# Optimization experiments

Measured on AMD Instinct MI355X. Metric: run time of the kernel, lower is better.

The kernel has to match this reference:

```python
import jax, jax.numpy as jnp
import numpy as np

EPS = 1e-6
PC_MIN = jnp.array([-50.0, -50.0, -4.0], jnp.float32)
PC_MAX = jnp.array([50.0, 50.0, 4.0], jnp.float32)
IMG_H, IMG_W = 256, 704
G, P, L, D = 1, 8, 4, 128


def _conv3x3(x, w, b):
    y = jax.lax.conv_general_dilated(x, w, (1, 1), ((1, 1), (1, 1)),
                                     dimension_numbers=('NCHW', 'OIHW', 'NCHW'))
    return y + b[None, :, None, None]


def _inorm(x):
    # InstanceNorm2d(affine=False), eps=1e-5, per-sample per-channel over (H,W)
    m = jnp.mean(x, axis=(2, 3), keepdims=True)
    v = jnp.var(x, axis=(2, 3), keepdims=True)
    return (x - m) * jax.lax.rsqrt(v + 1e-5)


def _bilinear(img, xy):
    # img: [H, W, C]; xy: [M, 2] in [0,1] (align_corners=False, zero padding)
    H, W, _ = img.shape
    px = xy[:, 0] * W - 0.5
    py = xy[:, 1] * H - 0.5
    x0 = jnp.floor(px)
    y0 = jnp.floor(py)
    wx = px - x0
    wy = py - y0
    x0 = x0.astype(jnp.int32)
    y0 = y0.astype(jnp.int32)

    def tap(xi, yi, w):
        ok = (xi >= 0) & (xi < W) & (yi >= 0) & (yi < H)
        v = img[jnp.clip(yi, 0, H - 1), jnp.clip(xi, 0, W - 1)]
        return v * (w * ok)[:, None]

    return (tap(x0, y0, (1 - wx) * (1 - wy)) + tap(x0 + 1, y0, wx * (1 - wy)) +
            tap(x0, y0 + 1, (1 - wx) * wy) + tap(x0 + 1, y0 + 1, wx * wy))


def _sampling_4d(pts, feats, scale_w, l2i):
    # pts: [B,Q,G,P,3]; feats: list of [B*G,N,Hl,Wl,C]; scale_w: [B,Q,G,1,P,L]; l2i: [B,N,4,4]
    B, Q, g, p, _ = pts.shape
    N = l2i.shape[1]
    hom = jnp.concatenate([pts, jnp.ones(pts.shape[:-1] + (1,), pts.dtype)], -1)
    cam = jnp.einsum('bnij,bqgpj->bqngpi', l2i, hom)  # project to each camera
    z = cam[..., 2:3]
    xy = cam[..., :2] / jnp.maximum(z, 1e-5)
    xy = xy / jnp.array([IMG_W, IMG_H], xy.dtype)
    xy = jnp.where(z > 1e-5, xy, -1e4)  # behind camera -> samples zero
    xy = jnp.transpose(xy, (0, 3, 2, 1, 4, 5)).reshape(B * g * N, Q * p, 2)
    out = 0.0
    for l, f in enumerate(feats):
        C = f.shape[-1]
        fi = f.reshape(B * g * N, f.shape[2], f.shape[3], C)
        s = jax.vmap(_bilinear)(fi, xy).reshape(B, g, N, Q, p, C).sum(2)  # sum over cameras
        w = jnp.transpose(scale_w[:, :, :, 0, :, l], (0, 2, 1, 3))  # [B,G,Q,P]
        out = out + s * w[..., None]
    return jnp.transpose(out, (0, 2, 1, 3, 4))  # [B,Q,G,P,C]


def _forward(feat0, feat1, feat2, feat3, lidar2img, bev_query, bev_pos,
             in_w, in_b, off_w, off_b, sw_w, sw_b,
             pe_w1, pe_b1, pe_w2, pe_b2,
             mid_w1, mid_b1, mid_w2, mid_b2, mid_w3, mid_b3,
             out_w, out_b):
    B, _, h, w = bev_query.shape
    # decoder prologue: b n (g c) H W -> (b g) n H W c  (G=1)
    feats = [jnp.transpose(f, (0, 1, 3, 4, 2)) for f in (feat0, feat1, feat2, feat3)]
    q = _inorm(bev_query + _conv3x3(bev_query, in_w, in_b))
    qf = jnp.transpose(q, (0, 2, 3, 1)).reshape(B, h * w, D)
    # sampling offsets (1x1 conv as matmul), mode='grid', scale=1.0
    off = jax.nn.sigmoid(qf @ off_w.T + off_b).reshape(B, h * w, G, P, 3)
    lim_xy = 0.25 * 1.0 + EPS
    lim_z = 4.0 + EPS
    off = jnp.concatenate([off[..., :2] * 2 * lim_xy - lim_xy,
                           off[..., 2:3] * 2 * lim_z - lim_z], -1)
    ref = bev_pos.reshape(B, h * w, 1, 1, 3) * (PC_MAX - PC_MIN) + PC_MIN
    pts = ref + off  # [B,Q,G,P,3] in world coords
    sw = (qf @ sw_w.T + sw_b).reshape(B, h * w, G, P, L)[:, :, :, None]  # b q g 1 p l
    sw = jax.nn.softmax(sw, axis=-1)
    sampled = _sampling_4d(pts, feats, sw, lidar2img)  # [B,Q,G,P,128]
    ref_n = (pts - PC_MIN) / (PC_MAX - PC_MIN)
    pe = jax.nn.relu(ref_n @ pe_w1 + pe_b1) @ pe_w2 + pe_b2  # PositionalEncodingMap MLP
    sampled = sampled + pe
    # b (h w) g p c -> b (p g c) h w
    sf = jnp.transpose(sampled, (0, 3, 2, 4, 1)).reshape(B, P * G * 128, h, w)
    m = jax.nn.gelu(jnp.einsum('oi,bihw->bohw', mid_w1, sf) + mid_b1[None, :, None, None], approximate=False)
    m = jax.nn.gelu(jnp.einsum('oi,bihw->bohw', mid_w2, m) + mid_b2[None, :, None, None], approximate=False)
    m = jnp.einsum('oi,bihw->bohw', mid_w3, m) + mid_b3[None, :, None, None]
    q = _inorm(q + m)
    q = _inorm(q + _conv3x3(q, out_w, out_b))
    height = jnp.transpose(off[..., 2], (0, 2, 3, 1)).reshape(B, G, P, h, w)
    return q, height


def _lidar2img_np():
    mats = []
    K = np.array([[500., 0., IMG_W / 2, 0.],
                  [0., 500., IMG_H / 2, 0.],
                  [0., 0., 1., 0.],
                  [0., 0., 0., 1.]])
    for n in range(6):
        th = 2 * np.pi * n / 6
        fwd = np.array([np.cos(th), np.sin(th), 0.])
        right = np.array([-np.sin(th), np.cos(th), 0.])
        down = np.array([0., 0., -1.])
        R = np.stack([right, down, fwd])
        c = fwd * 0.5 + np.array([0., 0., 1.5])
        T = np.eye(4)
        T[:3, :3] = R
        T[:3, 3] = -R @ c
        mats.append(K @ T)
    return np.stack(mats)[None].astype(np.float32)


def setup_inputs():
    key = jax.random.key(0)
    ks = jax.random.split(key, 16)

    def rn(k, shape, s=0.02):
        return jax.random.normal(k, shape, jnp.float32) * s

    B, N, h, w = 1, 6, 128, 128
    return dict(
        feat0=jax.random.normal(ks[0], (B, N, 128, 32, 88), jnp.float32),
        feat1=jax.random.normal(ks[1], (B, N, 128, 16, 44), jnp.float32),
        feat2=jax.random.normal(ks[2], (B, N, 128, 8, 22), jnp.float32),
        feat3=jax.random.normal(ks[3], (B, N, 128, 4, 11), jnp.float32),
        lidar2img=jnp.asarray(_lidar2img_np()),
        bev_query=jax.random.normal(ks[4], (B, 128, h, w), jnp.float32),
        bev_pos=jax.random.uniform(ks[5], (B, h, w, 3), jnp.float32),
        in_w=rn(ks[6], (128, 128, 3, 3)), in_b=jnp.zeros(128, jnp.float32),
        off_w=rn(ks[7], (G * P * 3, 128)),
        off_b=jax.random.uniform(ks[8], (G * P * 3,), jnp.float32, -4.0, 4.0),
        sw_w=rn(ks[9], (G * P * L, 128)), sw_b=jnp.zeros(G * P * L, jnp.float32),
        pe_w1=rn(ks[10], (3, 256), 0.5), pe_b1=jnp.zeros(256, jnp.float32),
        pe_w2=rn(ks[11], (256, 128), 0.1), pe_b2=jnp.zeros(128, jnp.float32),
        mid_w1=rn(ks[12], (512, P * 128)), mid_b1=jnp.zeros(512, jnp.float32),
        mid_w2=rn(ks[13], (512, 512)), mid_b2=jnp.zeros(512, jnp.float32),
        mid_w3=rn(ks[14], (128, 512)), mid_b3=jnp.zeros(128, jnp.float32),
        out_w=rn(ks[15], (128, 128, 3, 3)), out_b=jnp.zeros(128, jnp.float32),
    )


def reference(feat0, feat1, feat2, feat3, lidar2img, bev_query, bev_pos,
              in_w, in_b, off_w, off_b, sw_w, sw_b,
              pe_w1, pe_b1, pe_w2, pe_b2,
              mid_w1, mid_b1, mid_w2, mid_b2, mid_w3, mid_b3,
              out_w, out_b):
    return _forward(feat0, feat1, feat2, feat3, lidar2img, bev_query, bev_pos,
                    in_w, in_b, off_w, off_b, sw_w, sw_b,
                    pe_w1, pe_b1, pe_w2, pe_b2,
                    mid_w1, mid_b1, mid_w2, mid_b2, mid_w3, mid_b3,
                    out_w, out_b)
```

## Files before the change

### kernel.cpp

```cpp
#include <hip/hip_runtime.h>
#include <hip/hip_bf16.h>
#include <math.h>

#define HW 16384

typedef __attribute__((ext_vector_type(8))) short short8;
typedef __attribute__((ext_vector_type(4))) float floatx4;
typedef __attribute__((ext_vector_type(2))) float floatx2;

__device__ __forceinline__ float gelu_exact(float x){
    return 0.5f * x * (1.0f + erff(x * 0.7071067811865475f));
}

__device__ __forceinline__ floatx2 bf2x(unsigned int u){
    floatx2 r;
    r.x = __uint_as_float(u << 16);
    r.y = __uint_as_float(u & 0xffff0000u);
    return r;
}

__global__ __launch_bounds__(256) void feat_transpose_all_k(
    const float* __restrict__ f0, const float* __restrict__ f1,
    const float* __restrict__ f2, const float* __restrict__ f3,
    __hip_bfloat16* __restrict__ out)
{
    int idx = blockIdx.x * 256 + threadIdx.x;
    const float* in; int Hl, Wl, base;
    if (idx < 2162688)      { in = f0; Hl = 32; Wl = 88; base = 0; }
    else if (idx < 2703360) { in = f1; Hl = 16; Wl = 44; base = 2162688; }
    else if (idx < 2838528) { in = f2; Hl = 8;  Wl = 22; base = 2703360; }
    else                    { in = f3; Hl = 4;  Wl = 11; base = 2838528; }
    int r   = idx - base;
    int c   = r & 127;
    int pix = r >> 7;
    int x   = pix % Wl;
    int tt  = pix / Wl;
    int y   = tt % Hl;
    int n   = tt / Hl;
    out[idx] = __float2bfloat16(in[((n * 128 + c) * Hl + y) * Wl + x]);
}

__global__ __launch_bounds__(256) void prep_k(
    const float* __restrict__ mid_w1, const float* __restrict__ mid_w2,
    const float* __restrict__ mid_w3, const float* __restrict__ pe_w2,
    const float* __restrict__ off_w,  const float* __restrict__ off_b,
    const float* __restrict__ sw_w,   const float* __restrict__ sw_b,
    const float* __restrict__ in_w,   const float* __restrict__ out_w,
    __hip_bfloat16* __restrict__ Wb1, __hip_bfloat16* __restrict__ Wb2,
    __hip_bfloat16* __restrict__ Wb3, __hip_bfloat16* __restrict__ Wpe,
    __hip_bfloat16* __restrict__ Wof, float* __restrict__ Bof,
    __hip_bfloat16* __restrict__ Wcv1, __hip_bfloat16* __restrict__ Wcv2)
{
    int b = blockIdx.x, t = threadIdx.x;
    if (b < 2048) {
        int i = b * 256 + t; Wb1[i] = __float2bfloat16(mid_w1[i]);
    } else if (b < 3072) {
        int i = (b - 2048) * 256 + t; Wb2[i] = __float2bfloat16(mid_w2[i]);
    } else if (b < 3328) {
        int i = (b - 3072) * 256 + t; Wb3[i] = __float2bfloat16(mid_w3[i]);
    } else if (b < 3456) {
        int n = b - 3328; Wpe[n * 256 + t] = __float2bfloat16(pe_w2[t * 128 + n]);
    } else if (b < 3584) {
        int n = b - 3456;
        if (t < 128) {
            float w = 0.f;
            if (n < 24)      w = off_w[n * 128 + t];
            else if (n < 56) w = sw_w[(n - 24) * 128 + t];
            Wof[n * 128 + t] = __float2bfloat16(w);
            if (t == 0) Bof[n] = (n < 24) ? off_b[n] : ((n < 56) ? sw_b[n - 24] : 0.f);
        }
    } else if (b < 3712) {
        int o = b - 3584;
        for (int idx = t; idx < 1152; idx += 256) {
            int s = idx >> 7, i = idx & 127;
            Wcv1[o * 1152 + idx] = __float2bfloat16(in_w[(o * 128 + i) * 9 + s]);
        }
    } else {
        int o = b - 3712;
        for (int idx = t; idx < 1152; idx += 256) {
            int s = idx >> 7, i = idx & 127;
            Wcv2[o * 1152 + idx] = __float2bfloat16(out_w[(o * 128 + i) * 9 + s]);
        }
    }
}

__global__ __launch_bounds__(256) void chw2hwc_pad_k(
    const float* __restrict__ q, __hip_bfloat16* __restrict__ out)
{
    __shared__ float tile[128][65];
    int b = blockIdx.x;
    int y = b >> 1, x0 = (b & 1) * 64;
    int t = threadIdx.x;
    int xi = t & 63, c0 = t >> 6;
    for (int c = c0; c < 128; c += 4)
        tile[c][xi] = q[c * HW + y * 128 + x0 + xi];
    __syncthreads();
    int xp = t >> 2, cg = (t & 3) * 32;
    __hip_bfloat16* dst = out + ((size_t)(y + 1) * 130 + (x0 + 1 + xp)) * 128;
    #pragma unroll
    for (int g = 0; g < 4; g++) {
        int c = cg + g * 8;
        union { __hip_bfloat16 h[8]; uint4 u; } pk;
        #pragma unroll
        for (int j = 0; j < 8; j++) pk.h[j] = __float2bfloat16(tile[c + j][xp]);
        *(uint4*)&dst[c] = pk.u;
    }
}

template<int BM, int BN, int ACT, int OUTT, int CONV>
__global__ __launch_bounds__(256) void bgemm_k(
    const __hip_bfloat16* __restrict__ X, const __hip_bfloat16* __restrict__ W,
    const float* __restrict__ bias, void* __restrict__ outp,
    const float* __restrict__ res,
    int M, int K, int N)
{
    constexpr int ROWS = BM + BN;
    __shared__ __align__(16) __hip_bfloat16 SH[ROWS * 32];
    __hip_bfloat16* As = SH;
    __hip_bfloat16* Bs = SH + BM * 32;
    int t = threadIdx.x;
    int w = t >> 6, lane = t & 63;
    int mb = blockIdx.y * BM, nb = blockIdx.x * BN;
    int cy = mb >> 7, cx = mb & 127;
    constexpr int WM = BM / 2;
    constexpr int MI = WM / 16;
    constexpr int NJ = BN / 32;
    int wm = (w & 1) * WM, wn = (w >> 1) * (BN / 2);
    int lm = lane & 15, lq = lane >> 4;
    floatx4 zero = {0.f, 0.f, 0.f, 0.f};
    floatx4 acc[MI][NJ];
    #pragma unroll
    for (int i = 0; i < MI; i++)
        #pragma unroll
        for (int j = 0; j < NJ; j++) acc[i][j] = zero;
    constexpr int ITERS = (ROWS * 4) / 256;
    for (int kb = 0; kb < K; kb += 32) {
        int s = kb >> 7;
        int dyi = s / 3, dxi = s - dyi * 3;
        __syncthreads();
        #pragma unroll
        for (int it = 0; it < ITERS; it++) {
            int chunk = it * 256 + t;
            int row = chunk >> 2, ko = (chunk & 3) * 8;
            const __hip_bfloat16* src;
            if (row < BM) {
                if (CONV)
                    src = X + (((size_t)(cy + dyi) * 130) + (cx + dxi + row)) * 128 + (kb & 127) + ko;
                else
                    src = X + (size_t)(mb + row) * K + kb + ko;
            } else {
                src = W + (size_t)(nb + row - BM) * K + kb + ko;
            }
            __builtin_amdgcn_global_load_lds(
                (const __attribute__((address_space(1))) void*)src,
                (__attribute__((address_space(3))) void*)&SH[(size_t)(it * 256 + (t & ~63)) * 8],
                16, 0, 0);
        }
        __syncthreads();
        short8 af[MI], bf[NJ];
        #pragma unroll
        for (int i = 0; i < MI; i++)
            af[i] = *(const short8*)&As[(wm + i * 16 + lm) * 32 + lq * 8];
        #pragma unroll
        for (int j = 0; j < NJ; j++)
            bf[j] = *(const short8*)&Bs[(wn + j * 16 + lm) * 32 + lq * 8];
        #pragma unroll
        for (int i = 0; i < MI; i++)
            #pragma unroll
            for (int j = 0; j < NJ; j++)
                acc[i][j] = __builtin_amdgcn_mfma_f32_16x16x32_bf16(af[i], bf[j], acc[i][j], 0, 0, 0);
    }
    #pragma unroll
    for (int i = 0; i < MI; i++) {
        #pragma unroll
        for (int j = 0; j < NJ; j++) {
            int n = nb + wn + j * 16 + lm;
            float bv = bias[n];
            #pragma unroll
            for (int r = 0; r < 4; r++) {
                int m = mb + wm + i * 16 + lq * 4 + r;
                float v = acc[i][j][r] + bv;
                if (ACT) v = gelu_exact(v);
                if (OUTT == 0) {
                    ((__hip_bfloat16*)outp)[(size_t)m * N + n] = __float2bfloat16(v);
                } else {
                    if (res) v += res[(size_t)n * M + m];
                    ((float*)outp)[(size_t)n * M + m] = v;
                }
            }
        }
    }
}

__global__ __launch_bounds__(256) void pe_bgemm_k(
    const float* __restrict__ pts, const float* __restrict__ pe_w1,
    const float* __restrict__ pe_b1, const __hip_bfloat16* __restrict__ W,
    const float* __restrict__ bias, __hip_bfloat16* __restrict__ out)
{
    __shared__ __align__(16) __hip_bfloat16 As[128 * 32];
    __shared__ __align__(16) __hip_bfloat16 Bs[128 * 32];
    __shared__ __align__(16) float wps[4][256];
    int t = threadIdx.x;
    int w = t >> 6, lane = t & 63;
    int mb = blockIdx.x * 128;
    {
        int d = t >> 6, c = (t & 63) * 4;
        float4 v;
        if (d == 0) v = *(const float4*)&pe_b1[c];
        else        v = *(const float4*)&pe_w1[(d - 1) * 256 + c];
        *(float4*)&wps[d][c] = v;
    }
    int cg = t & 3;
    int r0 = t >> 2;
    float rn[2][3];
    #pragma unroll
    for (int h = 0; h < 2; h++) {
        int r = mb + r0 + h * 64;
        rn[h][0] = (pts[(size_t)r * 3 + 0] + 50.f) * 0.01f;
        rn[h][1] = (pts[(size_t)r * 3 + 1] + 50.f) * 0.01f;
        rn[h][2] = (pts[(size_t)r * 3 + 2] + 4.f) * 0.125f;
    }
    int wm = (w & 1) * 64, wn = (w >> 1) * 64;
    int lm = lane & 15, lq = lane >> 4;
    floatx4 zero = {0.f, 0.f, 0.f, 0.f};
    floatx4 acc[4][4];
    #pragma unroll
    for (int i = 0; i < 4; i++)
        #pragma unroll
        for (int j = 0; j < 4; j++) acc[i][j] = zero;
    for (int kb = 0; kb < 256; kb += 32) {
        __syncthreads();
        #pragma unroll
        for (int it = 0; it < 2; it++) {
            int chunk = it * 256 + t;
            int brow = chunk >> 2, ko = (chunk & 3) * 8;
            const __hip_bfloat16* src = W + (size_t)brow * 256 + kb + ko;
            __builtin_amdgcn_global_load_lds(
                (const __attribute__((address_space(1))) void*)src,
                (__attribute__((address_space(3))) void*)&Bs[(size_t)(it * 256 + (t & ~63)) * 8],
                16, 0, 0);
        }
        int c0 = kb + cg * 8;
        float4 bva = *(const float4*)&wps[0][c0], bvb = *(const float4*)&wps[0][c0 + 4];
        float4 wxa = *(const float4*)&wps[1][c0], wxb = *(const float4*)&wps[1][c0 + 4];
        float4 wya = *(const float4*)&wps[2][c0], wyb = *(const float4*)&wps[2][c0 + 4];
        float4 wza = *(const float4*)&wps[3][c0], wzb = *(const float4*)&wps[3][c0 + 4];
        #pragma unroll
        for (int h = 0; h < 2; h++) {
            const float* bv = (const float*)&bva;
            const float* wx = (const float*)&wxa;
            const float* wy = (const float*)&wya;
            const float* wz = (const float*)&wza;
            union { __hip_bfloat16 hh[8]; uint4 u; } pk;
            #pragma unroll
            for (int j = 0; j < 4; j++) {
                float v = bv[j] + rn[h][0] * wx[j] + rn[h][1] * wy[j] + rn[h][2] * wz[j];
                pk.hh[j] = __float2bfloat16(fmaxf(v, 0.f));
            }
            bv = (const float*)&bvb; wx = (const float*)&wxb;
            wy = (const float*)&wyb; wz = (const float*)&wzb;
            #pragma unroll
            for (int j = 0; j < 4; j++) {
                float v = bv[j] + rn[h][0] * wx[j] + rn[h][1] * wy[j] + rn[h][2] * wz[j];
                pk.hh[4 + j] = __float2bfloat16(fmaxf(v, 0.f));
            }
            *(uint4*)&As[(r0 + h * 64) * 32 + cg * 8] = pk.u;
        }
        __syncthreads();
        short8 af[4], bf[4];
        #pragma unroll
        for (int i = 0; i < 4; i++)
            af[i] = *(const short8*)&As[(wm + i * 16 + lm) * 32 + lq * 8];
        #pragma unroll
        for (int j = 0; j < 4; j++)
            bf[j] = *(const short8*)&Bs[(wn + j * 16 + lm) * 32 + lq * 8];
        #pragma unroll
        for (int i = 0; i < 4; i++)
            #pragma unroll
            for (int j = 0; j < 4; j++)
                acc[i][j] = __builtin_amdgcn_mfma_f32_16x16x32_bf16(af[i], bf[j], acc[i][j], 0, 0, 0);
    }
    #pragma unroll
    for (int i = 0; i < 4; i++) {
        #pragma unroll
        for (int j = 0; j < 4; j++) {
            int n = wn + j * 16 + lm;
            float bv = bias[n];
            #pragma unroll
            for (int r = 0; r < 4; r++) {
                int m = mb + wm + i * 16 + lq * 4 + r;
                out[(size_t)m * 128 + n] = __float2bfloat16(acc[i][j][r] + bv);
            }
        }
    }
}

__global__ __launch_bounds__(256) void inorm_k(
    const float* __restrict__ a, const float* __restrict__ addc, float* __restrict__ out)
{
    int c = blockIdx.x;
    const float* pa = a + (size_t)c * HW;
    const float* pb = addc ? addc + (size_t)c * HW : nullptr;
    const bool hasb = (pb != nullptr);
    float s = 0.f, s2 = 0.f;
    for (int i = threadIdx.x; i < HW; i += 256) {
        float v = hasb ? (pa[i] + pb[i]) : pa[i];
        s += v; s2 += v * v;
    }
    #pragma unroll
    for (int off = 32; off > 0; off >>= 1) {
        s  += __shfl_down(s,  off);
        s2 += __shfl_down(s2, off);
    }
    __shared__ float ls[4], ls2[4], stats[2];
    int wid = threadIdx.x >> 6, lane = threadIdx.x & 63;
    if (lane == 0) { ls[wid] = s; ls2[wid] = s2; }
    __syncthreads();
    if (threadIdx.x == 0) {
        float t = 0.f, t2 = 0.f;
        for (int i = 0; i < 4; i++) { t += ls[i]; t2 += ls2[i]; }
        float mean = t * (1.0f / HW);
        float var  = t2 * (1.0f / HW) - mean * mean;
        stats[0] = mean;
        stats[1] = rsqrtf(var + 1e-5f);
    }
    __syncthreads();
    float mean = stats[0], rstd = stats[1];
    float* po = out + (size_t)c * HW;
    for (int i = threadIdx.x; i < HW; i += 256) {
        float v = hasb ? (pa[i] + pb[i]) : pa[i];
        po[i] = (v - mean) * rstd;
    }
}

__global__ __launch_bounds__(256) void offpost_k(
    const float* __restrict__ raw, const float* __restrict__ bev_pos,
    float* __restrict__ pts, float* __restrict__ swn, float* __restrict__ height_out)
{
    int pix = blockIdx.x * 256 + threadIdx.x;
    const float pcmin[3] = {-50.f, -50.f, -4.f};
    const float rng[3]   = {100.f, 100.f, 8.f};
    float bp[3];
    #pragma unroll
    for (int d = 0; d < 3; d++) bp[d] = bev_pos[pix * 3 + d];
    #pragma unroll
    for (int p = 0; p < 8; p++) {
        #pragma unroll
        for (int d = 0; d < 3; d++) {
            float acc = raw[(p * 3 + d) * HW + pix];
            float sv = 1.f / (1.f + expf(-acc));
            float lim = (d == 2) ? (4.0f + 1e-6f) : (0.25f + 1e-6f);
            float offv = sv * 2.f * lim - lim;
            float refv = bp[d] * rng[d] + pcmin[d];
            pts[pix * 24 + p * 3 + d] = refv + offv;
            if (d == 2) height_out[p * HW + pix] = offv;
        }
        float r[4], m = -1e30f;
        #pragma unroll
        for (int l = 0; l < 4; l++) {
            r[l] = raw[(24 + p * 4 + l) * HW + pix];
            m = fmaxf(m, r[l]);
        }
        float sum = 0.f;
        #pragma unroll
        for (int l = 0; l < 4; l++) { r[l] = expf(r[l] - m); sum += r[l]; }
        float inv = 1.f / sum;
        #pragma unroll
        for (int l = 0; l < 4; l++) swn[pix * 32 + p * 4 + l] = r[l] * inv;
    }
}

__global__ __launch_bounds__(128) void sample_k(
    const __hip_bfloat16* __restrict__ featT, const float* __restrict__ pts,
    const float* __restrict__ swn,   const float* __restrict__ l2i,
    __hip_bfloat16* __restrict__ sf)
{
    int pix = blockIdx.x;
    int t = threadIdx.x;
    int lane = t & 63, wv = t >> 6;
    __shared__ float pts_s[24];
    __shared__ float swl_s[32];
    __shared__ float M[96];
    __shared__ __align__(16) int   offs[8][24][4];
    __shared__ __align__(16) float wts[8][24][4];
    __shared__ int cnt[8];
    if (t < 96) M[t] = l2i[t];
    if (t < 24) pts_s[t] = pts[pix * 24 + t];
    if (t < 32) swl_s[t] = swn[pix * 32 + t];
    if (t < 8)  cnt[t] = 0;
    __syncthreads();

    floatx2 acc[4];
    #pragma unroll
    for (int i = 0; i < 4; i++) {
        unsigned int u = *(const unsigned int*)&sf[(size_t)pix * 1024 + (wv * 4 + i) * 128 + 2 * lane];
        acc[i] = bf2x(u);
    }

    const int lHt[4] = {32, 16, 8, 4}, lWt[4] = {88, 44, 22, 11};
    const int loff[4] = {0, 2162688, 2703360, 2838528};
    for (int cb = t; cb < 192; cb += 128) {
        int p = cb / 24;
        int rr = cb - p * 24;
        int n = rr >> 2, l = rr & 3;
        float X = pts_s[p * 3], Y = pts_s[p * 3 + 1], Z = pts_s[p * 3 + 2];
        const float* Mn = &M[n * 16];
        float zc = Mn[8] * X + Mn[9] * Y + Mn[10] * Z + Mn[11];
        if (zc > 1e-5f) {
            float inv = 1.f / zc;
            float xn = (Mn[0] * X + Mn[1] * Y + Mn[2] * Z + Mn[3]) * inv * (1.f / 704.f);
            float yn = (Mn[4] * X + Mn[5] * Y + Mn[6] * Z + Mn[7]) * inv * (1.f / 256.f);
            int Wl = lWt[l], Hl = lHt[l];
            float px = xn * Wl - 0.5f, py = yn * Hl - 0.5f;
            px = fminf(fmaxf(px, -2.f), (float)(Wl + 1));
            py = fminf(fmaxf(py, -2.f), (float)(Hl + 1));
            float x0f = floorf(px), y0f = floorf(py);
            float wx = px - x0f, wy = py - y0f;
            int x0 = (int)x0f, y0 = (int)y0f;
            bool xi0 = (unsigned)x0 < (unsigned)Wl, xi1 = (unsigned)(x0 + 1) < (unsigned)Wl;
            bool yi0 = (unsigned)y0 < (unsigned)Hl, yi1 = (unsigned)(y0 + 1) < (unsigned)Hl;
            if ((xi0 || xi1) && (yi0 || yi1)) {
                float wl = swl_s[p * 4 + l];
                float w00 = wl * (1.f - wx) * (1.f - wy) * (float)(xi0 && yi0);
                float w10 = wl * wx * (1.f - wy)         * (float)(xi1 && yi0);
                float w01 = wl * (1.f - wx) * wy         * (float)(xi0 && yi1);
                float w11 = wl * wx * wy                 * (float)(xi1 && yi1);
                int x0c = min(max(x0, 0), Wl - 1), x1c = min(max(x0 + 1, 0), Wl - 1);
                int y0c = min(max(y0, 0), Hl - 1), y1c = min(max(y0 + 1, 0), Hl - 1);
                int base = loff[l] + n * Hl * Wl * 128;
                int idx = atomicAdd(&cnt[p], 1);
                offs[p][idx][0] = base + (y0c * Wl + x0c) * 128;
                offs[p][idx][1] = base + (y0c * Wl + x1c) * 128;
                offs[p][idx][2] = base + (y1c * Wl + x0c) * 128;
                offs[p][idx][3] = base + (y1c * Wl + x1c) * 128;
                wts[p][idx][0] = w00; wts[p][idx][1] = w10;
                wts[p][idx][2] = w01; wts[p][idx][3] = w11;
            }
        }
    }
    __syncthreads();

    #pragma unroll 1
    for (int i = 0; i < 4; i++) {
        int p = wv * 4 + i;
        int np = cnt[p];
        floatx2 a = acc[i];
        #pragma unroll 1
        for (int j = 0; j < np; j++) {
            int4   o = *(const int4*)&offs[p][j][0];
            float4 w = *(const float4*)&wts[p][j][0];
            unsigned int v0 = ((const unsigned int*)(featT + o.x))[lane];
            unsigned int v1 = ((const unsigned int*)(featT + o.y))[lane];
            unsigned int v2 = ((const unsigned int*)(featT + o.z))[lane];
            unsigned int v3 = ((const unsigned int*)(featT + o.w))[lane];
            a += bf2x(v0) * w.x;
            a += bf2x(v1) * w.y;
            a += bf2x(v2) * w.z;
            a += bf2x(v3) * w.w;
        }
        acc[i] = a;
    }
    #pragma unroll
    for (int i = 0; i < 4; i++) {
        union { __hip_bfloat16 h[2]; unsigned int u; } pk;
        pk.h[0] = __float2bfloat16(acc[i].x);
        pk.h[1] = __float2bfloat16(acc[i].y);
        *(unsigned int*)&sf[(size_t)pix * 1024 + (wv * 4 + i) * 128 + 2 * lane] = pk.u;
    }
}

extern "C" void kernel_launch(void* const* d_in, const int* in_sizes, int n_in,
                              void* d_out, int out_size, void* d_ws, size_t ws_size,
                              hipStream_t stream)
{
    const float* feat[4] = {(const float*)d_in[0], (const float*)d_in[1],
                            (const float*)d_in[2], (const float*)d_in[3]};
    const float* l2i       = (const float*)d_in[4];
    const float* bev_query = (const float*)d_in[5];
    const float* bev_pos   = (const float*)d_in[6];
    const float* in_w  = (const float*)d_in[7];  const float* in_b  = (const float*)d_in[8];
    const float* off_w = (const float*)d_in[9];  const float* off_b = (const float*)d_in[10];
    const float* sw_w  = (const float*)d_in[11]; const float* sw_b  = (const float*)d_in[12];
    const float* pe_w1 = (const float*)d_in[13]; const float* pe_b1 = (const float*)d_in[14];
    const float* pe_w2 = (const float*)d_in[15]; const float* pe_b2 = (const float*)d_in[16];
    const float* mid_w1 = (const float*)d_in[17]; const float* mid_b1 = (const float*)d_in[18];
    const float* mid_w2 = (const float*)d_in[19]; const float* mid_b2 = (const float*)d_in[20];
    const float* mid_w3 = (const float*)d_in[21]; const float* mid_b3 = (const float*)d_in[22];
    const float* out_w  = (const float*)d_in[23]; const float* out_b  = (const float*)d_in[24];

    float* ws = (float*)d_ws;
    float* fTf = ws;
    __hip_bfloat16* fT = (__hip_bfloat16*)fTf;
    float* Bb  = fTf + 1436160;
    float* Cb  = Bb + 2097152;
    float* Gb  = Cb + 2097152;
    float* Dp  = Gb + 2097152;
    float* Eb  = Dp + 393216;
    float* QTf = Eb + 524288;
    __hip_bfloat16* qT = (__hip_bfloat16*)QTf;
    float* SFf = QTf + 1081600;
    __hip_bfloat16* sfb = (__hip_bfloat16*)SFf;
    float* M1f = SFf + 8388608;
    __hip_bfloat16* m1b = (__hip_bfloat16*)M1f;
    float* M2f = M1f + 4194304;
    __hip_bfloat16* m2b = (__hip_bfloat16*)M2f;
    float* WC1 = M2f + 4194304;
    __hip_bfloat16* Wcv1 = (__hip_bfloat16*)WC1;
    float* WC2 = WC1 + 73728;
    __hip_bfloat16* Wcv2 = (__hip_bfloat16*)WC2;
    float* W1f = WC2 + 73728;
    __hip_bfloat16* Wb1 = (__hip_bfloat16*)W1f;
    float* W2f = W1f + 262144;
    __hip_bfloat16* Wb2 = (__hip_bfloat16*)W2f;
    float* W3f = W2f + 131072;
    __hip_bfloat16* Wb3 = (__hip_bfloat16*)W3f;
    float* WPf = W3f + 32768;
    __hip_bfloat16* Wpe = (__hip_bfloat16*)WPf;
    float* WOf = WPf + 16384;
    __hip_bfloat16* Wof = (__hip_bfloat16*)WOf;
    float* Bof = WOf + 8192;

    float* q_out = (float*)d_out;
    float* h_out = q_out + 2097152;

    hipMemsetAsync(qT, 0, (size_t)130 * 130 * 128 * sizeof(__hip_bfloat16), stream);

    feat_transpose_all_k<<<11220, 256, 0, stream>>>(feat[0], feat[1], feat[2], feat[3], fT);
    prep_k<<<3840, 256, 0, stream>>>(mid_w1, mid_w2, mid_w3, pe_w2, off_w, off_b, sw_w, sw_b,
                                     in_w, out_w, Wb1, Wb2, Wb3, Wpe, Wof, Bof, Wcv1, Wcv2);

    chw2hwc_pad_k<<<256, 256, 0, stream>>>(bev_query, qT);
    bgemm_k<64, 64, 0, 1, 1><<<dim3(2, 256), 256, 0, stream>>>(qT, Wcv1, in_b, Bb, bev_query, HW, 1152, 128);
    inorm_k<<<128, 256, 0, stream>>>(Bb, nullptr, Cb);

    chw2hwc_pad_k<<<256, 256, 0, stream>>>(Cb, qT);
    bgemm_k<64, 64, 0, 1, 1><<<dim3(2, 256), 256, 0, stream>>>(qT + 131 * 128, Wof, Bof, Bb, nullptr, HW, 128, 128);
    offpost_k<<<64, 256, 0, stream>>>(Bb, bev_pos, Dp, Eb, h_out);

    pe_bgemm_k<<<1024, 256, 0, stream>>>(Dp, pe_w1, pe_b1, Wpe, pe_b2, sfb);

    sample_k<<<HW, 128, 0, stream>>>(fT, Dp, Eb, l2i, sfb);

    bgemm_k<128, 128, 1, 0, 0><<<dim3(4, 128), 256, 0, stream>>>(sfb, Wb1, mid_b1, m1b, nullptr, HW, 1024, 512);
    bgemm_k<128, 128, 1, 0, 0><<<dim3(4, 128), 256, 0, stream>>>(m1b, Wb2, mid_b2, m2b, nullptr, HW, 512, 512);
    bgemm_k<64, 64, 0, 1, 0><<<dim3(2, 256), 256, 0, stream>>>(m2b, Wb3, mid_b3, Bb, Cb, HW, 512, 128);
    inorm_k<<<128, 256, 0, stream>>>(Bb, nullptr, Gb);

    chw2hwc_pad_k<<<256, 256, 0, stream>>>(Gb, qT);
    bgemm_k<64, 64, 0, 1, 1><<<dim3(2, 256), 256, 0, stream>>>(qT, Wcv2, out_b, Cb, Gb, HW, 1152, 128);
    inorm_k<<<128, 256, 0, stream>>>(Cb, nullptr, q_out);
}
```

Before: 442.7 us.

## Fuse instance-norm statistics into GEMM epilogues and widen sampling kernel

The GEMM epilogue now accumulates per-channel sum and sum-of-squares via atomics. Normalization is applied lazily in the following transpose/pad kernel or the residual read, which removes three standalone inorm passes and leaves a cheap vectorized apply only at the end. Separately, sample_k moves to 256 threads per pixel with 2 points per wave and unrolls the tap loop by two for more memory-level parallelism. The trade-off is atomic contention on the stats buffers and E[x²]−mean² variance computed from float atomics, which can be less accurate and order-dependent.

```diff
diff --git a/kernel.cpp b/kernel.cpp
--- a/kernel.cpp
+++ b/kernel.cpp
@@ -85,12 +85,24 @@
 }
 
 __global__ __launch_bounds__(256) void chw2hwc_pad_k(
-    const float* __restrict__ q, __hip_bfloat16* __restrict__ out)
+    const float* __restrict__ q, const float* __restrict__ stats,
+    __hip_bfloat16* __restrict__ out)
 {
     __shared__ float tile[128][65];
+    __shared__ float sm[128], sr[128];
+    int t = threadIdx.x;
+    if (t < 128) {
+        if (stats) {
+            float s = stats[2 * t], s2 = stats[2 * t + 1];
+            float mean = s * (1.0f / HW);
+            sm[t] = mean;
+            sr[t] = rsqrtf(s2 * (1.0f / HW) - mean * mean + 1e-5f);
+        } else {
+            sm[t] = 0.f; sr[t] = 1.f;
+        }
+    }
     int b = blockIdx.x;
     int y = b >> 1, x0 = (b & 1) * 64;
-    int t = threadIdx.x;
     int xi = t & 63, c0 = t >> 6;
     for (int c = c0; c < 128; c += 4)
         tile[c][xi] = q[c * HW + y * 128 + x0 + xi];
@@ -102,7 +114,8 @@
         int c = cg + g * 8;
         union { __hip_bfloat16 h[8]; uint4 u; } pk;
         #pragma unroll
-        for (int j = 0; j < 8; j++) pk.h[j] = __float2bfloat16(tile[c + j][xp]);
+        for (int j = 0; j < 8; j++)
+            pk.h[j] = __float2bfloat16((tile[c + j][xp] - sm[c + j]) * sr[c + j]);
         *(uint4*)&dst[c] = pk.u;
     }
 }
@@ -112,6 +125,7 @@
     const __hip_bfloat16* __restrict__ X, const __hip_bfloat16* __restrict__ W,
     const float* __restrict__ bias, void* __restrict__ outp,
     const float* __restrict__ res,
+    const float* __restrict__ rstats, float* __restrict__ ostats,
     int M, int K, int N)
 {
     constexpr int ROWS = BM + BN;
@@ -170,12 +184,20 @@
             for (int j = 0; j < NJ; j++)
                 acc[i][j] = __builtin_amdgcn_mfma_f32_16x16x32_bf16(af[i], bf[j], acc[i][j], 0, 0, 0);
     }
-    #pragma unroll
-    for (int i = 0; i < MI; i++) {
-        #pragma unroll
-        for (int j = 0; j < NJ; j++) {
-            int n = nb + wn + j * 16 + lm;
-            float bv = bias[n];
+    float invM = 1.0f / (float)M;
+    #pragma unroll
+    for (int j = 0; j < NJ; j++) {
+        int n = nb + wn + j * 16 + lm;
+        float bv = bias[n];
+        float rmean = 0.f, rrstd = 0.f;
+        if (OUTT == 1 && res && rstats) {
+            float s = rstats[2 * n], s2 = rstats[2 * n + 1];
+            rmean = s * invM;
+            rrstd = rsqrtf(s2 * invM - rmean * rmean + 1e-5f);
+        }
+        float ss = 0.f, ss2 = 0.f;
+        #pragma unroll
+        for (int i = 0; i < MI; i++) {
             #pragma unroll
             for (int r = 0; r < 4; r++) {
                 int m = mb + wm + i * 16 + lq * 4 + r;
@@ -184,9 +206,21 @@
                 if (OUTT == 0) {
                     ((__hip_bfloat16*)outp)[(size_t)m * N + n] = __float2bfloat16(v);
                 } else {
-                    if (res) v += res[(size_t)n * M + m];
+                    if (res) {
+                        float rv = res[(size_t)n * M + m];
+                        v += rstats ? (rv - rmean) * rrstd : rv;
+                    }
                     ((float*)outp)[(size_t)n * M + m] = v;
+                    ss += v; ss2 += v * v;
                 }
+            }
+        }
+        if (OUTT == 1 && ostats) {
+            ss  += __shfl_xor(ss, 16);  ss  += __shfl_xor(ss, 32);
+            ss2 += __shfl_xor(ss2, 16); ss2 += __shfl_xor(ss2, 32);
+            if (lq == 0) {
+                atomicAdd(&ostats[2 * n], ss);
+                atomicAdd(&ostats[2 * n + 1], ss2);
             }
         }
     }
@@ -295,41 +329,23 @@
     }
 }
 
-__global__ __launch_bounds__(256) void inorm_k(
-    const float* __restrict__ a, const float* __restrict__ addc, float* __restrict__ out)
-{
-    int c = blockIdx.x;
-    const float* pa = a + (size_t)c * HW;
-    const float* pb = addc ? addc + (size_t)c * HW : nullptr;
-    const bool hasb = (pb != nullptr);
-    float s = 0.f, s2 = 0.f;
-    for (int i = threadIdx.x; i < HW; i += 256) {
-        float v = hasb ? (pa[i] + pb[i]) : pa[i];
-        s += v; s2 += v * v;
-    }
-    #pragma unroll
-    for (int off = 32; off > 0; off >>= 1) {
-        s  += __shfl_down(s,  off);
-        s2 += __shfl_down(s2, off);
-    }
-    __shared__ float ls[4], ls2[4], stats[2];
-    int wid = threadIdx.x >> 6, lane = threadIdx.x & 63;
-    if (lane == 0) { ls[wid] = s; ls2[wid] = s2; }
-    __syncthreads();
-    if (threadIdx.x == 0) {
-        float t = 0.f, t2 = 0.f;
-        for (int i = 0; i < 4; i++) { t += ls[i]; t2 += ls2[i]; }
-        float mean = t * (1.0f / HW);
-        float var  = t2 * (1.0f / HW) - mean * mean;
-        stats[0] = mean;
-        stats[1] = rsqrtf(var + 1e-5f);
-    }
-    __syncthreads();
-    float mean = stats[0], rstd = stats[1];
-    float* po = out + (size_t)c * HW;
-    for (int i = threadIdx.x; i < HW; i += 256) {
-        float v = hasb ? (pa[i] + pb[i]) : pa[i];
-        po[i] = (v - mean) * rstd;
+__global__ __launch_bounds__(256) void inorm_apply_k(
+    const float* __restrict__ in, const float* __restrict__ stats, float* __restrict__ out)
+{
+    int b = blockIdx.x;
+    int c = b >> 3, seg = b & 7;
+    float s = stats[2 * c], s2 = stats[2 * c + 1];
+    float mean = s * (1.0f / HW);
+    float rstd = rsqrtf(s2 * (1.0f / HW) - mean * mean + 1e-5f);
+    const float4* pi = (const float4*)(in + (size_t)c * HW + seg * 2048);
+    float4*       po = (float4*)(out + (size_t)c * HW + seg * 2048);
+    int t = threadIdx.x;
+    #pragma unroll
+    for (int k = 0; k < 2; k++) {
+        float4 v = pi[t + k * 256];
+        v.x = (v.x - mean) * rstd; v.y = (v.y - mean) * rstd;
+        v.z = (v.z - mean) * rstd; v.w = (v.w - mean) * rstd;
+        po[t + k * 256] = v;
     }
 }
 
@@ -370,7 +386,7 @@
     }
 }
 
-__global__ __launch_bounds__(128) void sample_k(
+__global__ __launch_bounds__(256) void sample_k(
     const __hip_bfloat16* __restrict__ featT, const float* __restrict__ pts,
     const float* __restrict__ swn,   const float* __restrict__ l2i,
     __hip_bfloat16* __restrict__ sf)
@@ -390,18 +406,18 @@
     if (t < 8)  cnt[t] = 0;
     __syncthreads();
 
-    floatx2 acc[4];
-    #pragma unroll
-    for (int i = 0; i < 4; i++) {
-        unsigned int u = *(const unsigned int*)&sf[(size_t)pix * 1024 + (wv * 4 + i) * 128 + 2 * lane];
+    floatx2 acc[2];
+    #pragma unroll
+    for (int i = 0; i < 2; i++) {
+        unsigned int u = *(const unsigned int*)&sf[(size_t)pix * 1024 + (wv * 2 + i) * 128 + 2 * lane];
         acc[i] = bf2x(u);
     }
 
     const int lHt[4] = {32, 16, 8, 4}, lWt[4] = {88, 44, 22, 11};
     const int loff[4] = {0, 2162688, 2703360, 2838528};
-    for (int cb = t; cb < 192; cb += 128) {
-        int p = cb / 24;
-        int rr = cb - p * 24;
+    if (t < 192) {
+        int p = t / 24;
+        int rr = t - p * 24;
         int n = rr >> 2, l = rr & 3;
         float X = pts_s[p * 3], Y = pts_s[p * 3 + 1], Z = pts_s[p * 3 + 2];
         const float* Mn = &M[n * 16];
@@ -429,10 +445,10 @@
                 int y0c = min(max(y0, 0), Hl - 1), y1c = min(max(y0 + 1, 0), Hl - 1);
                 int base = loff[l] + n * Hl * Wl * 128;
                 int idx = atomicAdd(&cnt[p], 1);
-                offs[p][idx][0] = base + (y0c * Wl + x0c) * 128;
-                offs[p][idx][1] = base + (y0c * Wl + x1c) * 128;
-                offs[p][idx][2] = base + (y1c * Wl + x0c) * 128;
-                offs[p][idx][3] = base + (y1c * Wl + x1c) * 128;
+                offs[p][idx][0] = (base + (y0c * Wl + x0c) * 128) * 2;
+                offs[p][idx][1] = (base + (y0c * Wl + x1c) * 128) * 2;
+                offs[p][idx][2] = (base + (y1c * Wl + x0c) * 128) * 2;
+                offs[p][idx][3] = (base + (y1c * Wl + x1c) * 128) * 2;
                 wts[p][idx][0] = w00; wts[p][idx][1] = w10;
                 wts[p][idx][2] = w01; wts[p][idx][3] = w11;
             }
@@ -440,32 +456,58 @@
     }
     __syncthreads();
 
-    #pragma unroll 1
-    for (int i = 0; i < 4; i++) {
-        int p = wv * 4 + i;
+    const char* fbase = (const char*)featT;
+    int lane4 = lane * 4;
+    #pragma unroll
+    for (int i = 0; i < 2; i++) {
+        int p = wv * 2 + i;
         int np = cnt[p];
-        floatx2 a = acc[i];
+        floatx2 a0 = acc[i];
+        floatx2 a1 = {0.f, 0.f};
+        int j = 0;
         #pragma unroll 1
-        for (int j = 0; j < np; j++) {
+        for (; j + 2 <= np; j += 2) {
+            int4   oA = *(const int4*)&offs[p][j][0];
+            float4 wA = *(const float4*)&wts[p][j][0];
+            int4   oB = *(const int4*)&offs[p][j + 1][0];
+            float4 wB = *(const float4*)&wts[p][j + 1][0];
+            unsigned int v0 = *(const unsigned int*)(fbase + (unsigned)(oA.x + lane4));
+            unsigned int v1 = *(const unsigned int*)(fbase + (unsigned)(oA.y + lane4));
+            unsigned int v2 = *(const unsigned int*)(fbase + (unsigned)(oA.z + lane4));
+            unsigned int v3 = *(const unsigned int*)(fbase + (unsigned)(oA.w + lane4));
+            unsigned int v4 = *(const unsigned int*)(fbase + (unsigned)(oB.x + lane4));
+            unsigned int v5 = *(const unsigned int*)(fbase + (unsigned)(oB.y + lane4));
+            unsigned int v6 = *(const unsigned int*)(fbase + (unsigned)(oB.z + lane4));
+            unsigned int v7 = *(const unsigned int*)(fbase + (unsigned)(oB.w + lane4));
+            a0 += bf2x(v0) * wA.x;
+            a0 += bf2x(v1) * wA.y;
+            a0 += bf2x(v2) * wA.z;
+            a0 += bf2x(v3) * wA.w;
+            a1 += bf2x(v4) * wB.x;
+            a1 += bf2x(v5) * wB.y;
+            a1 += bf2x(v6) * wB.z;
+            a1 += bf2x(v7) * wB.w;
+        }
+        if (j < np) {
             int4   o = *(const int4*)&offs[p][j][0];
             float4 w = *(const float4*)&wts[p][j][0];
-            unsigned int v0 = ((const unsigned int*)(featT + o.x))[lane];
-            unsigned int v1 = ((const unsigned int*)(featT + o.y))[lane];
-            unsigned int v2 = ((const unsigned int*)(featT + o.z))[lane];
-            unsigned int v3 = ((const unsigned int*)(featT + o.w))[lane];
-            a += bf2x(v0) * w.x;
-            a += bf2x(v1) * w.y;
-            a += bf2x(v2) * w.z;
-            a += bf2x(v3) * w.w;
-        }
-        acc[i] = a;
-    }
-    #pragma unroll
-    for (int i = 0; i < 4; i++) {
+            unsigned int v0 = *(const unsigned int*)(fbase + (unsigned)(o.x + lane4));
+            unsigned int v1 = *(const unsigned int*)(fbase + (unsigned)(o.y + lane4));
+            unsigned int v2 = *(const unsigned int*)(fbase + (unsigned)(o.z + lane4));
+            unsigned int v3 = *(const unsigned int*)(fbase + (unsigned)(o.w + lane4));
+            a0 += bf2x(v0) * w.x;
+            a0 += bf2x(v1) * w.y;
+            a0 += bf2x(v2) * w.z;
+            a0 += bf2x(v3) * w.w;
+        }
+        acc[i] = a0 + a1;
+    }
+    #pragma unroll
+    for (int i = 0; i < 2; i++) {
         union { __hip_bfloat16 h[2]; unsigned int u; } pk;
         pk.h[0] = __float2bfloat16(acc[i].x);
         pk.h[1] = __float2bfloat16(acc[i].y);
-        *(unsigned int*)&sf[(size_t)pix * 1024 + (wv * 4 + i) * 128 + 2 * lane] = pk.u;
+        *(unsigned int*)&sf[(size_t)pix * 1024 + (wv * 2 + i) * 128 + 2 * lane] = pk.u;
     }
 }
 
@@ -519,34 +561,43 @@
     float* WOf = WPf + 16384;
     __hip_bfloat16* Wof = (__hip_bfloat16*)WOf;
     float* Bof = WOf + 8192;
+    float* Stats = Bof + 128;
+    float* stats1 = Stats;
+    float* stats2 = Stats + 256;
+    float* stats3 = Stats + 512;
 
     float* q_out = (float*)d_out;
     float* h_out = q_out + 2097152;
 
     hipMemsetAsync(qT, 0, (size_t)130 * 130 * 128 * sizeof(__hip_bfloat16), stream);
+    hipMemsetAsync(Stats, 0, 768 * sizeof(float), stream);
 
     feat_transpose_all_k<<<11220, 256, 0, stream>>>(feat[0], feat[1], feat[2], feat[3], fT);
     prep_k<<<3840, 256, 0, stream>>>(mid_w1, mid_w2, mid_w3, pe_w2, off_w, off_b, sw_w, sw_b,
                                      in_w, out_w, Wb1, Wb2, Wb3, Wpe, Wof, Bof, Wcv1, Wcv2);
 
-    chw2hwc_pad_k<<<256, 256, 0, stream>>>(bev_query, qT);
-    bgemm_k<64, 64, 0, 1, 1><<<dim3(2, 256), 256, 0, stream>>>(qT, Wcv1, in_b, Bb, bev_query, HW, 1152, 128);
-    inorm_k<<<128, 256, 0, stream>>>(Bb, nullptr, Cb);
-
-    chw2hwc_pad_k<<<256, 256, 0, stream>>>(Cb, qT);
-    bgemm_k<64, 64, 0, 1, 1><<<dim3(2, 256), 256, 0, stream>>>(qT + 131 * 128, Wof, Bof, Bb, nullptr, HW, 128, 128);
+    chw2hwc_pad_k<<<256, 256, 0, stream>>>(bev_query, nullptr, qT);
+    bgemm_k<64, 64, 0, 1, 1><<<dim3(2, 256), 256, 0, stream>>>(
+        qT, Wcv1, in_b, Cb, bev_query, nullptr, stats1, HW, 1152, 128);
+
+    chw2hwc_pad_k<<<256, 256, 0, stream>>>(Cb, stats1, qT);
+    bgemm_k<64, 64, 0, 1, 1><<<dim3(2, 256), 256, 0, stream>>>(
+        qT + 131 * 128, Wof, Bof, Bb, nullptr, nullptr, nullptr, HW, 128, 128);
     offpost_k<<<64, 256, 0, stream>>>(Bb, bev_pos, Dp, Eb, h_out);
 
     pe_bgemm_k<<<1024, 256, 0, stream>>>(Dp, pe_w1, pe_b1, Wpe, pe_b2, sfb);
 
-    sample_k<<<HW, 128, 0, stream>>>(fT, Dp, Eb, l2i, sfb);
-
-    bgemm_k<128, 128, 1, 0, 0><<<dim3(4, 128), 256, 0, stream>>>(sfb, Wb1, mid_b1, m1b, nullptr, HW, 1024, 512);
-    bgemm_k<128, 128, 1, 0, 0><<<dim3(4, 128), 256, 0, stream>>>(m1b, Wb2, mid_b2, m2b, nullptr, HW, 512, 512);
-    bgemm_k<64, 64, 0, 1, 0><<<dim3(2, 256), 256, 0, stream>>>(m2b, Wb3, mid_b3, Bb, Cb, HW, 512, 128);
-    inorm_k<<<128, 256, 0, stream>>>(Bb, nullptr, Gb);
-
-    chw2hwc_pad_k<<<256, 256, 0, stream>>>(Gb, qT);
-    bgemm_k<64, 64, 0, 1, 1><<<dim3(2, 256), 256, 0, stream>>>(qT, Wcv2, out_b, Cb, Gb, HW, 1152, 128);
-    inorm_k<<<128, 256, 0, stream>>>(Cb, nullptr, q_out);
-}
+    sample_k<<<HW, 256, 0, stream>>>(fT, Dp, Eb, l2i, sfb);
+
+    bgemm_k<128, 128, 1, 0, 0><<<dim3(4, 128), 256, 0, stream>>>(
+        sfb, Wb1, mid_b1, m1b, nullptr, nullptr, nullptr, HW, 1024, 512);
+    bgemm_k<128, 128, 1, 0, 0><<<dim3(4, 128), 256, 0, stream>>>(
+        m1b, Wb2, mid_b2, m2b, nullptr, nullptr, nullptr, HW, 512, 512);
+    bgemm_k<64, 64, 0, 1, 0><<<dim3(2, 256), 256, 0, stream>>>(
+        m2b, Wb3, mid_b3, Bb, Cb, stats1, stats2, HW, 512, 128);
+
+    chw2hwc_pad_k<<<256, 256, 0, stream>>>(Bb, stats2, qT);
+    bgemm_k<64, 64, 0, 1, 1><<<dim3(2, 256), 256, 0, stream>>>(
+        qT, Wcv2, out_b, Gb, Bb, stats2, stats3, HW, 1152, 128);
+    inorm_apply_k<<<1024, 256, 0, stream>>>(Gb, stats3, q_out);
+}
```

New measurement: 427.7 us. 3.4% less time.
